# Optimization experiments

Measured on AMD Instinct MI355X. Metric: run time of the kernel, lower is better.

## Reference

```python
import jax, jax.numpy as jnp
import numpy as np

N = 170000      # nodes (ogbn-arxiv scale)
E = 2720000     # edges (avg degree 16)
IN, H, L, OUT = 128, 256, 4, 40
BN_EPS = 1e-5


def setup_inputs() -> dict:
    key = jax.random.key(0)
    ks = jax.random.split(key, 6)
    x = jax.random.normal(ks[0], (N, IN), jnp.float32)
    edge_index = jax.random.randint(ks[1], (2, E), 0, N, dtype=jnp.int64)
    W_in = jax.random.normal(ks[2], (IN, H), jnp.float32) * 0.05
    b_in = jnp.zeros((H,), jnp.float32)
    W_hid = jax.random.normal(ks[3], (L - 1, H, H), jnp.float32) * 0.05
    b_hid = jnp.zeros((L - 1, H), jnp.float32)
    gamma = jnp.ones((L, H), jnp.float32)
    beta = jnp.zeros((L, H), jnp.float32)
    W_out = jax.random.normal(ks[4], (L * H, OUT), jnp.float32) * 0.05
    b_out = jnp.zeros((OUT,), jnp.float32)
    return dict(x=x, edge_index=edge_index, W_in=W_in, b_in=b_in,
                W_hid=W_hid, b_hid=b_hid, gamma=gamma, beta=beta,
                W_out=W_out, b_out=b_out)


def _gcn_aggregate(h, src, dst, norm_e, inv_deg):
    # message passing with symmetric normalization + self-loop term
    msg = h[src] * norm_e[:, None]                      # [E, H] gather
    agg = jax.ops.segment_sum(msg, dst, num_segments=N)  # [N, H] scatter-add
    return agg + h * inv_deg[:, None]                   # self-loop: deg^-1


def reference(x, edge_index, W_in, b_in, W_hid, b_hid, gamma, beta, W_out, b_out):
    src, dst = edge_index[0], edge_index[1]
    # degree (incl. self-loop), PyG gcn_norm style
    deg = jax.ops.segment_sum(jnp.ones((E,), x.dtype), dst, num_segments=N) + 1.0
    dinv = jax.lax.rsqrt(deg)
    norm_e = dinv[src] * dinv[dst]
    inv_deg = 1.0 / deg

    outs = []
    h = x
    for i in range(L):
        W = W_in if i == 0 else W_hid[i - 1]
        b = b_in if i == 0 else b_hid[i - 1]
        h = _gcn_aggregate(h @ W, src, dst, norm_e, inv_deg) + b
        # BatchNorm1d (training-mode batch statistics, biased variance)
        mean = jnp.mean(h, axis=0)
        var = jnp.mean(jnp.square(h - mean), axis=0)
        h = (h - mean) * jax.lax.rsqrt(var + BN_EPS) * gamma[i] + beta[i]
        h = jax.nn.relu(h)  # dropout is identity in eval mode
        outs.append(h)

    z = jnp.concatenate(outs, axis=-1) @ W_out + b_out  # JK 'cat' -> [N, L*H] @ [L*H, OUT]
    return jax.nn.log_softmax(z, axis=-1)
```

## Files before the change

### kernel.cpp

```cpp
#include <hip/hip_runtime.h>
#include <math.h>

constexpr int kN = 170000;
constexpr int kE = 2720000;
constexpr int kFin = 128;
constexpr int kFh = 256;
constexpr int kL = 4;
constexpr int kFout = 40;

typedef __attribute__((ext_vector_type(8))) short bf16x8;
typedef __attribute__((ext_vector_type(4))) float f32x4;

__device__ __forceinline__ float jk_b2f(unsigned short u) {
    unsigned int x = ((unsigned int)u) << 16;
    float f;
    __builtin_memcpy(&f, &x, 4);
    return f;
}
__device__ __forceinline__ unsigned short jk_f2b(float f) {
    unsigned int x;
    __builtin_memcpy(&x, &f, 4);
    unsigned int r = (x + 0x7fffu + ((x >> 16) & 1u)) >> 16;
    return (unsigned short)r;
}

union U4 {
    uint4 v;
    unsigned short s[8];
};

__global__ void jk6_zero_i(int* p, int n) {
    int i = blockIdx.x * blockDim.x + threadIdx.x;
    if (i < n) p[i] = 0;
}
__global__ void jk6_zero_f(float* p, int n) {
    int i = blockIdx.x * blockDim.x + threadIdx.x;
    if (i < n) p[i] = 0.0f;
}

__global__ void jk6_detect(const int* eb, int* flag) {
    __shared__ int nz;
    if (threadIdx.x == 0) nz = 0;
    __syncthreads();
    int bad = 0;
    for (int j = 0; j < 4; j++) {
        int idx = threadIdx.x * 4 + j;
        if (eb[2 * idx + 1] != 0) bad = 1;
    }
    if (bad) atomicOr(&nz, 1);
    __syncthreads();
    if (threadIdx.x == 0) {
        flag[0] = nz ? 0 : 1;
        flag[1] = 0;
    }
}

__global__ void jk6_count(const int* eb, const int* flag, int* counts, int* rank) {
    int e = blockIdx.x * blockDim.x + threadIdx.x;
    if (e >= kE) return;
    int s64 = flag[0];
    int d = eb[(kE + e) << s64];
    rank[e] = atomicAdd(&counts[d], 1);
}

__global__ void jk6_nodeprep(const int* counts, float* dinv, float* invdeg, int* off,
                             int* cursor) {
    int n = blockIdx.x * blockDim.x + threadIdx.x;
    if (n < kN) {
        int c = counts[n];
        float deg = (float)c + 1.0f;
        dinv[n] = rsqrtf(deg);
        invdeg[n] = 1.0f / deg;
        off[n] = atomicAdd(cursor, c);
    }
}

__global__ void jk6_fill(const int* eb, const int* flag, const int* rank, const int* off,
                         const float* dinv, int* csr_src, float* csr_w) {
    int e = blockIdx.x * blockDim.x + threadIdx.x;
    if (e >= kE) return;
    int s64 = flag[0];
    int s = eb[e << s64];
    int d = eb[(kE + e) << s64];
    int p = off[d] + rank[e];
    csr_src[p] = s;
    csr_w[p] = dinv[s] * dinv[d];
}

__global__ void jk6_wt(const float* W, unsigned short* Wt, int K) {
    int idx = blockIdx.x * blockDim.x + threadIdx.x;
    if (idx >= K * kFh) return;
    int c = idx / K, k = idx % K;
    Wt[idx] = jk_f2b(W[(size_t)k * kFh + c]);
}

__global__ void jk6_wtout(const float* Wout, unsigned short* Wto) {
    int idx = blockIdx.x * blockDim.x + threadIdx.x;
    if (idx >= kL * 48 * 256) return;
    int l = idx / (48 * 256);
    int rem = idx % (48 * 256);
    int col = rem >> 8, k = rem & 255;
    float wv = (col < kFout) ? Wout[(size_t)(l * kFh + k) * kFout + col] : 0.f;
    unsigned short hi = jk_f2b(wv);
    float res = wv - jk_b2f(hi);
    unsigned short lo = jk_f2b(res);
    Wto[((size_t)(l * 2 + 0) * 48 + col) * 256 + k] = hi;
    Wto[((size_t)(l * 2 + 1) * 48 + col) * 256 + k] = lo;
}

template <int AF32>
__global__ __launch_bounds__(256) void jk6_gemm(const void* Aptr, const unsigned short* Wt,
                                                unsigned short* C, int K) {
    __shared__ unsigned short As[128][40];
    __shared__ unsigned short Bs[128][40];
    int tid = threadIdx.x;
    int row0 = blockIdx.x * 128;
    int n0 = blockIdx.y * 128;
    int lane = tid & 63, w = tid >> 6;
    int wm = w >> 1, wn = w & 1;
    int lr = lane & 15, lg = lane >> 4;

    f32x4 acc[4][4];
#pragma unroll
    for (int i = 0; i < 4; i++)
#pragma unroll
        for (int j = 0; j < 4; j++) acc[i][j] = (f32x4){0.f, 0.f, 0.f, 0.f};

    int sr = tid >> 1;
    int skh = (tid & 1) * 16;

    for (int k0 = 0; k0 < K; k0 += 32) {
        {
            int row = row0 + sr;
            if (AF32) {
                const float* A = (const float*)Aptr;
                unsigned short tmp[16];
                if (row < kN) {
                    const float* g = A + (size_t)row * K + k0 + skh;
#pragma unroll
                    for (int j = 0; j < 16; j++) tmp[j] = jk_f2b(g[j]);
                } else {
#pragma unroll
                    for (int j = 0; j < 16; j++) tmp[j] = 0;
                }
                *(uint4*)&As[sr][skh] = *(uint4*)&tmp[0];
                *(uint4*)&As[sr][skh + 8] = *(uint4*)&tmp[8];
            } else {
                const unsigned short* A = (const unsigned short*)Aptr;
                uint4 u0 = make_uint4(0, 0, 0, 0), u1 = make_uint4(0, 0, 0, 0);
                if (row < kN) {
                    const unsigned short* g = A + (size_t)row * K + k0 + skh;
                    u0 = *(const uint4*)g;
                    u1 = *(const uint4*)(g + 8);
                }
                *(uint4*)&As[sr][skh] = u0;
                *(uint4*)&As[sr][skh + 8] = u1;
            }
        }
        {
            const unsigned short* g = Wt + (size_t)(n0 + sr) * K + k0 + skh;
            *(uint4*)&Bs[sr][skh] = *(const uint4*)g;
            *(uint4*)&Bs[sr][skh + 8] = *(const uint4*)(g + 8);
        }
        __syncthreads();

        bf16x8 af[4], bfr[4];
#pragma unroll
        for (int mi = 0; mi < 4; mi++)
            af[mi] = *(const bf16x8*)&As[wm * 64 + mi * 16 + lr][lg * 8];
#pragma unroll
        for (int ni = 0; ni < 4; ni++)
            bfr[ni] = *(const bf16x8*)&Bs[wn * 64 + ni * 16 + lr][lg * 8];
#pragma unroll
        for (int mi = 0; mi < 4; mi++)
#pragma unroll
            for (int ni = 0; ni < 4; ni++)
                acc[mi][ni] = __builtin_amdgcn_mfma_f32_16x16x32_bf16(af[mi], bfr[ni],
                                                                      acc[mi][ni], 0, 0, 0);
        __syncthreads();
    }

#pragma unroll
    for (int mi = 0; mi < 4; mi++) {
#pragma unroll
        for (int j = 0; j < 4; j++) {
            int row = row0 + wm * 64 + mi * 16 + lg * 4 + j;
            if (row < kN) {
#pragma unroll
                for (int ni = 0; ni < 4; ni++) {
                    int col = n0 + wn * 64 + ni * 16 + lr;
                    C[(size_t)row * kFh + col] = jk_f2b(acc[mi][ni][j]);
                }
            }
        }
    }
}

__global__ __launch_bounds__(256) void jk6_agg(const unsigned short* t, const float* bias,
                                               const int* off, const int* cnt, const int* csr_src,
                                               const float* csr_w, const float* invdeg,
                                               unsigned short* h) {
    int n = blockIdx.x * 4 + (threadIdx.x >> 6);
    if (n >= kN) return;
    int l = threadIdx.x & 63;
    int half = l >> 5;
    int c0 = (l & 31) * 8;

    float acc[8];
    {
        U4 u;
        u.v = *(const uint4*)(t + (size_t)n * kFh + c0);
        float sw = half ? 0.0f : invdeg[n];
#pragma unroll
        for (int j = 0; j < 8; j++) acc[j] = sw * jk_b2f(u.s[j]);
    }

    int base = off[n], c = cnt[n];
    for (int i = 0; i < c; i += 8) {
        int e0 = i + half * 4;
        float w[4];
        U4 uu[4];
#pragma unroll
        for (int q = 0; q < 4; q++) {
            int e = e0 + q;
            bool v = e < c;
            int idx = v ? base + e : base;
            int src = csr_src[idx];
            w[q] = v ? csr_w[idx] : 0.0f;
            uu[q].v = *(const uint4*)(t + (size_t)src * kFh + c0);
        }
#pragma unroll
        for (int q = 0; q < 4; q++)
#pragma unroll
            for (int j = 0; j < 8; j++) acc[j] += w[q] * jk_b2f(uu[q].s[j]);
    }

#pragma unroll
    for (int j = 0; j < 8; j++) acc[j] += __shfl_xor(acc[j], 32, 64);

    if (half == 0) {
        U4 o;
#pragma unroll
        for (int j = 0; j < 8; j++) o.s[j] = jk_f2b(acc[j] + bias[c0 + j]);
        *(uint4*)(h + (size_t)n * kFh + c0) = o.v;
    }
}

__global__ __launch_bounds__(256) void jk6_bnstats(const unsigned short* h, float* stats) {
    __shared__ float lsum[256], lsq[256];
    int tid = threadIdx.x;
    lsum[tid] = 0.f;
    lsq[tid] = 0.f;
    __syncthreads();
    int c0 = (tid & 31) * 8;
    int grp = tid >> 5;
    float rs[8] = {}, rq[8] = {};
    for (int n = blockIdx.x * 8 + grp; n < kN; n += gridDim.x * 8) {
        U4 u;
        u.v = *(const uint4*)(h + (size_t)n * kFh + c0);
#pragma unroll
        for (int j = 0; j < 8; j++) {
            float v = jk_b2f(u.s[j]);
            rs[j] += v;
            rq[j] += v * v;
        }
    }
#pragma unroll
    for (int j = 0; j < 8; j++) {
        atomicAdd(&lsum[c0 + j], rs[j]);
        atomicAdd(&lsq[c0 + j], rq[j]);
    }
    __syncthreads();
    atomicAdd(&stats[tid], lsum[tid]);
    atomicAdd(&stats[256 + tid], lsq[tid]);
}

__global__ void jk6_bnfinal(const float* stats, const float* gamma, const float* beta, int layer,
                            float* scale, float* shift) {
    int c = threadIdx.x;
    float mean = stats[c] / (float)kN;
    float var = stats[256 + c] / (float)kN - mean * mean;
    var = var < 0.f ? 0.f : var;
    float sc = gamma[layer * kFh + c] * rsqrtf(var + 1e-5f);
    scale[c] = sc;
    shift[c] = beta[layer * kFh + c] - mean * sc;
}

template <int FIRST, int LAST>
__global__ __launch_bounds__(256) void jk6_zacc(unsigned short* h, const float* scale,
                                                const float* shift, const unsigned short* Wto,
                                                const float* bout, float* z, float* out) {
    __shared__ unsigned short Bs[2][48][264];
    __shared__ unsigned short As[128][40];
    __shared__ float ssc[256], ssh[256];
    int tid = threadIdx.x;
    for (int f = tid; f < 2 * 48 * 256; f += 256) {
        int hl = f / (48 * 256);
        int rem = f % (48 * 256);
        Bs[hl][rem >> 8][rem & 255] = Wto[f];
    }
    ssc[tid] = scale[tid];
    ssh[tid] = shift[tid];
    __syncthreads();

    int row0 = blockIdx.x * 128;
    int w = tid >> 6, lane = tid & 63;
    int lr = lane & 15, lg = lane >> 4;
    int sr = tid >> 1, skh = (tid & 1) * 16;

    f32x4 acc[2][3];
#pragma unroll
    for (int mi = 0; mi < 2; mi++)
#pragma unroll
        for (int ni = 0; ni < 3; ni++) acc[mi][ni] = (f32x4){0.f, 0.f, 0.f, 0.f};

    for (int k0 = 0; k0 < kFh; k0 += 32) {
        int row = row0 + sr;
        U4 o0, o1;
        if (row < kN) {
            U4 u0, u1;
            const unsigned short* g = h + (size_t)row * kFh + k0 + skh;
            u0.v = *(const uint4*)g;
            u1.v = *(const uint4*)(g + 8);
#pragma unroll
            for (int j = 0; j < 8; j++) {
                float v = jk_b2f(u0.s[j]) * ssc[k0 + skh + j] + ssh[k0 + skh + j];
                o0.s[j] = jk_f2b(v > 0.f ? v : 0.f);
            }
#pragma unroll
            for (int j = 0; j < 8; j++) {
                float v = jk_b2f(u1.s[j]) * ssc[k0 + skh + 8 + j] + ssh[k0 + skh + 8 + j];
                o1.s[j] = jk_f2b(v > 0.f ? v : 0.f);
            }
            if (!LAST) {
                *(uint4*)(h + (size_t)row * kFh + k0 + skh) = o0.v;
                *(uint4*)(h + (size_t)row * kFh + k0 + skh + 8) = o1.v;
            }
        } else {
#pragma unroll
            for (int j = 0; j < 8; j++) { o0.s[j] = 0; o1.s[j] = 0; }
        }
        *(uint4*)&As[sr][skh] = o0.v;
        *(uint4*)&As[sr][skh + 8] = o1.v;
        __syncthreads();

        bf16x8 af[2], bh[3], bl[3];
#pragma unroll
        for (int mi = 0; mi < 2; mi++)
            af[mi] = *(const bf16x8*)&As[w * 32 + mi * 16 + lr][lg * 8];
#pragma unroll
        for (int ni = 0; ni < 3; ni++) {
            bh[ni] = *(const bf16x8*)&Bs[0][ni * 16 + lr][k0 + lg * 8];
            bl[ni] = *(const bf16x8*)&Bs[1][ni * 16 + lr][k0 + lg * 8];
        }
#pragma unroll
        for (int mi = 0; mi < 2; mi++)
#pragma unroll
            for (int ni = 0; ni < 3; ni++) {
                acc[mi][ni] = __builtin_amdgcn_mfma_f32_16x16x32_bf16(af[mi], bh[ni],
                                                                      acc[mi][ni], 0, 0, 0);
                acc[mi][ni] = __builtin_amdgcn_mfma_f32_16x16x32_bf16(af[mi], bl[ni],
                                                                      acc[mi][ni], 0, 0, 0);
            }
        __syncthreads();
    }

#pragma unroll
    for (int mi = 0; mi < 2; mi++) {
#pragma unroll
        for (int j = 0; j < 4; j++) {
            int row = row0 + w * 32 + mi * 16 + lg * 4 + j;
            if (row >= kN) continue;
            if (!LAST) {
#pragma unroll
                for (int ni = 0; ni < 3; ni++) {
                    int col = ni * 16 + lr;
                    if (col < kFout) {
                        if (FIRST)
                            z[(size_t)row * kFout + col] = acc[mi][ni][j] + bout[col];
                        else
                            z[(size_t)row * kFout + col] += acc[mi][ni][j];
                    }
                }
            } else {
                const float* zp = z + (size_t)row * kFout;
                float v0 = zp[lr] + acc[mi][0][j];
                float v1 = zp[16 + lr] + acc[mi][1][j];
                float v2 = (lr < 8) ? (zp[32 + lr] + acc[mi][2][j]) : -1e30f;
                float m = fmaxf(fmaxf(v0, v1), v2);
                m = fmaxf(m, __shfl_xor(m, 1, 64));
                m = fmaxf(m, __shfl_xor(m, 2, 64));
                m = fmaxf(m, __shfl_xor(m, 4, 64));
                m = fmaxf(m, __shfl_xor(m, 8, 64));
                float s = expf(v0 - m) + expf(v1 - m) + ((lr < 8) ? expf(v2 - m) : 0.f);
                s += __shfl_xor(s, 1, 64);
                s += __shfl_xor(s, 2, 64);
                s += __shfl_xor(s, 4, 64);
                s += __shfl_xor(s, 8, 64);
                float ls = m + logf(s);
                float* op = out + (size_t)row * kFout;
                op[lr] = v0 - ls;
                op[16 + lr] = v1 - ls;
                if (lr < 8) op[32 + lr] = v2 - ls;
            }
        }
    }
}

extern "C" void kernel_launch(void* const* d_in, const int* in_sizes, int n_in,
                              void* d_out, int out_size, void* d_ws, size_t ws_size,
                              hipStream_t stream) {
    (void)in_sizes; (void)n_in; (void)out_size; (void)ws_size;
    const float* x = (const float*)d_in[0];
    const int* eb = (const int*)d_in[1];
    const float* W_in = (const float*)d_in[2];
    const float* b_in = (const float*)d_in[3];
    const float* W_hid = (const float*)d_in[4];
    const float* b_hid = (const float*)d_in[5];
    const float* gamma = (const float*)d_in[6];
    const float* beta = (const float*)d_in[7];
    const float* W_out = (const float*)d_in[8];
    const float* b_out = (const float*)d_in[9];
    float* out = (float*)d_out;

    char* p = (char*)d_ws;
    auto alloc = [&](size_t b) -> void* {
        void* r = (void*)p;
        p += (b + 255) & ~(size_t)255;
        return r;
    };
    int* flag = (int*)alloc(8);
    int* counts = (int*)alloc((size_t)kN * 4);
    int* off = (int*)alloc((size_t)kN * 4);
    float* dinv = (float*)alloc((size_t)kN * 4);
    float* invdeg = (float*)alloc((size_t)kN * 4);
    float* bnsums = (float*)alloc((size_t)kL * 512 * 4);
    float* bnss = (float*)alloc((size_t)kL * 512 * 4);
    int* rank = (int*)alloc((size_t)kE * 4);
    int* csr_src = (int*)alloc((size_t)kE * 4);
    float* csr_w = (float*)alloc((size_t)kE * 4);
    unsigned short* hA = (unsigned short*)alloc((size_t)kN * kFh * 2);
    unsigned short* hB = (unsigned short*)alloc((size_t)kN * kFh * 2);
    float* z = (float*)alloc((size_t)kN * kFout * 4);
    unsigned short* Wt0 = (unsigned short*)alloc((size_t)kFin * kFh * 2);
    unsigned short* Wt1 = (unsigned short*)alloc((size_t)kFh * kFh * 2);
    unsigned short* Wt2 = (unsigned short*)alloc((size_t)kFh * kFh * 2);
    unsigned short* Wt3 = (unsigned short*)alloc((size_t)kFh * kFh * 2);
    unsigned short* Wto = (unsigned short*)alloc((size_t)kL * 2 * 48 * 256 * 2);

    jk6_zero_i<<<(kN + 255) / 256, 256, 0, stream>>>(counts, kN);
    jk6_zero_f<<<(kL * 512 + 255) / 256, 256, 0, stream>>>(bnsums, kL * 512);
    jk6_detect<<<1, 256, 0, stream>>>(eb, flag);
    jk6_count<<<(kE + 255) / 256, 256, 0, stream>>>(eb, flag, counts, rank);
    jk6_nodeprep<<<(kN + 255) / 256, 256, 0, stream>>>(counts, dinv, invdeg, off, flag + 1);
    jk6_fill<<<(kE + 255) / 256, 256, 0, stream>>>(eb, flag, rank, off, dinv, csr_src, csr_w);

    jk6_wt<<<(kFin * kFh + 255) / 256, 256, 0, stream>>>(W_in, Wt0, kFin);
    jk6_wt<<<(kFh * kFh + 255) / 256, 256, 0, stream>>>(W_hid, Wt1, kFh);
    jk6_wt<<<(kFh * kFh + 255) / 256, 256, 0, stream>>>(W_hid + (size_t)kFh * kFh, Wt2, kFh);
    jk6_wt<<<(kFh * kFh + 255) / 256, 256, 0, stream>>>(W_hid + (size_t)2 * kFh * kFh, Wt3, kFh);
    jk6_wtout<<<(kL * 48 * 256 + 255) / 256, 256, 0, stream>>>(W_out, Wto);

    unsigned short* Wts[4] = {Wt0, Wt1, Wt2, Wt3};
    dim3 gg((kN + 127) / 128, 2);
    int zg = (kN + 127) / 128;
    for (int l = 0; l < kL; l++) {
        const float* b = (l == 0) ? b_in : b_hid + (size_t)(l - 1) * kFh;
        int K = (l == 0) ? kFin : kFh;
        if (l == 0)
            jk6_gemm<1><<<gg, 256, 0, stream>>>(x, Wts[l], hA, K);
        else
            jk6_gemm<0><<<gg, 256, 0, stream>>>(hB, Wts[l], hA, K);
        jk6_agg<<<(kN + 3) / 4, 256, 0, stream>>>(hA, b, off, counts, csr_src, csr_w, invdeg, hB);
        jk6_bnstats<<<1024, 256, 0, stream>>>(hB, bnsums + (size_t)l * 512);
        jk6_bnfinal<<<1, 256, 0, stream>>>(bnsums + (size_t)l * 512, gamma, beta, l,
                                           bnss + (size_t)l * 512, bnss + (size_t)l * 512 + 256);
        const unsigned short* wtl = Wto + (size_t)l * 2 * 48 * 256;
        float* sc = bnss + (size_t)l * 512;
        if (l == 0)
            jk6_zacc<1, 0><<<zg, 256, 0, stream>>>(hB, sc, sc + 256, wtl, b_out, z, out);
        else if (l < kL - 1)
            jk6_zacc<0, 0><<<zg, 256, 0, stream>>>(hB, sc, sc + 256, wtl, b_out, z, out);
        else
            jk6_zacc<0, 1><<<zg, 256, 0, stream>>>(hB, sc, sc + 256, wtl, b_out, z, out);
    }
}
```

Measured before the change: 1.802 ms.

## Fuse BN+ReLU into next GEMM load, pack CSR edges, one node per half-wave

The zacc kernel no longer writes the normalized, ReLU'd activations back to h. Instead the next layer's GEMM applies the BN scale/shift and ReLU while loading A tiles, which removes a full N×256 bf16 write per layer. Edge source index and weight are packed into one int2 array, so each edge needs a single 8-byte load. Aggregation now gives each node 32 lanes that walk all of its edges, dropping the two-half split and the cross-half shuffle reduction. This costs some extra ALU work in the GEMM prologue and gives less memory-level parallelism per node in aggregation.

```diff
diff --git a/kernel.cpp b/kernel.cpp
--- a/kernel.cpp
+++ b/kernel.cpp
@@ -29,16 +29,16 @@
     unsigned short s[8];
 };
 
-__global__ void jk6_zero_i(int* p, int n) {
+__global__ void jk7_zero_i(int* p, int n) {
     int i = blockIdx.x * blockDim.x + threadIdx.x;
     if (i < n) p[i] = 0;
 }
-__global__ void jk6_zero_f(float* p, int n) {
+__global__ void jk7_zero_f(float* p, int n) {
     int i = blockIdx.x * blockDim.x + threadIdx.x;
     if (i < n) p[i] = 0.0f;
 }
 
-__global__ void jk6_detect(const int* eb, int* flag) {
+__global__ void jk7_detect(const int* eb, int* flag) {
     __shared__ int nz;
     if (threadIdx.x == 0) nz = 0;
     __syncthreads();
@@ -55,7 +55,7 @@
     }
 }
 
-__global__ void jk6_count(const int* eb, const int* flag, int* counts, int* rank) {
+__global__ void jk7_count(const int* eb, const int* flag, int* counts, int* rank) {
     int e = blockIdx.x * blockDim.x + threadIdx.x;
     if (e >= kE) return;
     int s64 = flag[0];
@@ -63,7 +63,7 @@
     rank[e] = atomicAdd(&counts[d], 1);
 }
 
-__global__ void jk6_nodeprep(const int* counts, float* dinv, float* invdeg, int* off,
+__global__ void jk7_nodeprep(const int* counts, float* dinv, float* invdeg, int* off,
                              int* cursor) {
     int n = blockIdx.x * blockDim.x + threadIdx.x;
     if (n < kN) {
@@ -75,26 +75,26 @@
     }
 }
 
-__global__ void jk6_fill(const int* eb, const int* flag, const int* rank, const int* off,
-                         const float* dinv, int* csr_src, float* csr_w) {
+__global__ void jk7_fill(const int* eb, const int* flag, const int* rank, const int* off,
+                         const float* dinv, int2* csr) {
     int e = blockIdx.x * blockDim.x + threadIdx.x;
     if (e >= kE) return;
     int s64 = flag[0];
     int s = eb[e << s64];
     int d = eb[(kE + e) << s64];
     int p = off[d] + rank[e];
-    csr_src[p] = s;
-    csr_w[p] = dinv[s] * dinv[d];
-}
-
-__global__ void jk6_wt(const float* W, unsigned short* Wt, int K) {
+    float w = dinv[s] * dinv[d];
+    csr[p] = make_int2(s, __float_as_int(w));
+}
+
+__global__ void jk7_wt(const float* W, unsigned short* Wt, int K) {
     int idx = blockIdx.x * blockDim.x + threadIdx.x;
     if (idx >= K * kFh) return;
     int c = idx / K, k = idx % K;
     Wt[idx] = jk_f2b(W[(size_t)k * kFh + c]);
 }
 
-__global__ void jk6_wtout(const float* Wout, unsigned short* Wto) {
+__global__ void jk7_wtout(const float* Wout, unsigned short* Wto) {
     int idx = blockIdx.x * blockDim.x + threadIdx.x;
     if (idx >= kL * 48 * 256) return;
     int l = idx / (48 * 256);
@@ -108,12 +108,19 @@
     Wto[((size_t)(l * 2 + 1) * 48 + col) * 256 + k] = lo;
 }
 
-template <int AF32>
-__global__ __launch_bounds__(256) void jk6_gemm(const void* Aptr, const unsigned short* Wt,
-                                                unsigned short* C, int K) {
+template <int MODE>
+__global__ __launch_bounds__(256) void jk7_gemm(const void* Aptr, const unsigned short* Wt,
+                                                unsigned short* C, int K, const float* sc,
+                                                const float* sh) {
     __shared__ unsigned short As[128][40];
     __shared__ unsigned short Bs[128][40];
+    __shared__ float ssc[256], ssh[256];
     int tid = threadIdx.x;
+    if (MODE == 1) {
+        ssc[tid] = sc[tid];
+        ssh[tid] = sh[tid];
+    }
+    __syncthreads();
     int row0 = blockIdx.x * 128;
     int n0 = blockIdx.y * 128;
     int lane = tid & 63, w = tid >> 6;
@@ -132,7 +139,7 @@
     for (int k0 = 0; k0 < K; k0 += 32) {
         {
             int row = row0 + sr;
-            if (AF32) {
+            if (MODE == 0) {
                 const float* A = (const float*)Aptr;
                 unsigned short tmp[16];
                 if (row < kN) {
@@ -147,14 +154,28 @@
                 *(uint4*)&As[sr][skh + 8] = *(uint4*)&tmp[8];
             } else {
                 const unsigned short* A = (const unsigned short*)Aptr;
-                uint4 u0 = make_uint4(0, 0, 0, 0), u1 = make_uint4(0, 0, 0, 0);
+                U4 o0, o1;
                 if (row < kN) {
+                    U4 u0, u1;
                     const unsigned short* g = A + (size_t)row * K + k0 + skh;
-                    u0 = *(const uint4*)g;
-                    u1 = *(const uint4*)(g + 8);
+                    u0.v = *(const uint4*)g;
+                    u1.v = *(const uint4*)(g + 8);
+#pragma unroll
+                    for (int j = 0; j < 8; j++) {
+                        float v = jk_b2f(u0.s[j]) * ssc[k0 + skh + j] + ssh[k0 + skh + j];
+                        o0.s[j] = jk_f2b(v > 0.f ? v : 0.f);
+                    }
+#pragma unroll
+                    for (int j = 0; j < 8; j++) {
+                        float v = jk_b2f(u1.s[j]) * ssc[k0 + skh + 8 + j] + ssh[k0 + skh + 8 + j];
+                        o1.s[j] = jk_f2b(v > 0.f ? v : 0.f);
+                    }
+                } else {
+#pragma unroll
+                    for (int j = 0; j < 8; j++) { o0.s[j] = 0; o1.s[j] = 0; }
                 }
-                *(uint4*)&As[sr][skh] = u0;
-                *(uint4*)&As[sr][skh + 8] = u1;
+                *(uint4*)&As[sr][skh] = o0.v;
+                *(uint4*)&As[sr][skh + 8] = o1.v;
             }
         }
         {
@@ -196,38 +217,33 @@
     }
 }
 
-__global__ __launch_bounds__(256) void jk6_agg(const unsigned short* t, const float* bias,
-                                               const int* off, const int* cnt, const int* csr_src,
-                                               const float* csr_w, const float* invdeg,
-                                               unsigned short* h) {
-    int n = blockIdx.x * 4 + (threadIdx.x >> 6);
+__global__ __launch_bounds__(256) void jk7_agg(const unsigned short* t, const float* bias,
+                                               const int* off, const int* cnt, const int2* csr,
+                                               const float* invdeg, unsigned short* h) {
+    int n = blockIdx.x * 8 + (threadIdx.x >> 5);
     if (n >= kN) return;
-    int l = threadIdx.x & 63;
-    int half = l >> 5;
-    int c0 = (l & 31) * 8;
+    int c0 = (threadIdx.x & 31) * 8;
 
     float acc[8];
     {
         U4 u;
         u.v = *(const uint4*)(t + (size_t)n * kFh + c0);
-        float sw = half ? 0.0f : invdeg[n];
+        float sw = invdeg[n];
 #pragma unroll
         for (int j = 0; j < 8; j++) acc[j] = sw * jk_b2f(u.s[j]);
     }
 
     int base = off[n], c = cnt[n];
-    for (int i = 0; i < c; i += 8) {
-        int e0 = i + half * 4;
+    for (int i = 0; i < c; i += 4) {
         float w[4];
         U4 uu[4];
 #pragma unroll
         for (int q = 0; q < 4; q++) {
-            int e = e0 + q;
+            int e = i + q;
             bool v = e < c;
-            int idx = v ? base + e : base;
-            int src = csr_src[idx];
-            w[q] = v ? csr_w[idx] : 0.0f;
-            uu[q].v = *(const uint4*)(t + (size_t)src * kFh + c0);
+            int2 cw = csr[v ? base + e : base];
+            w[q] = v ? __int_as_float(cw.y) : 0.0f;
+            uu[q].v = *(const uint4*)(t + (size_t)cw.x * kFh + c0);
         }
 #pragma unroll
         for (int q = 0; q < 4; q++)
@@ -235,18 +251,13 @@
             for (int j = 0; j < 8; j++) acc[j] += w[q] * jk_b2f(uu[q].s[j]);
     }
 
-#pragma unroll
-    for (int j = 0; j < 8; j++) acc[j] += __shfl_xor(acc[j], 32, 64);
-
-    if (half == 0) {
-        U4 o;
-#pragma unroll
-        for (int j = 0; j < 8; j++) o.s[j] = jk_f2b(acc[j] + bias[c0 + j]);
-        *(uint4*)(h + (size_t)n * kFh + c0) = o.v;
-    }
-}
-
-__global__ __launch_bounds__(256) void jk6_bnstats(const unsigned short* h, float* stats) {
+    U4 o;
+#pragma unroll
+    for (int j = 0; j < 8; j++) o.s[j] = jk_f2b(acc[j] + bias[c0 + j]);
+    *(uint4*)(h + (size_t)n * kFh + c0) = o.v;
+}
+
+__global__ __launch_bounds__(256) void jk7_bnstats(const unsigned short* h, float* stats) {
     __shared__ float lsum[256], lsq[256];
     int tid = threadIdx.x;
     lsum[tid] = 0.f;
@@ -275,7 +286,7 @@
     atomicAdd(&stats[256 + tid], lsq[tid]);
 }
 
-__global__ void jk6_bnfinal(const float* stats, const float* gamma, const float* beta, int layer,
+__global__ void jk7_bnfinal(const float* stats, const float* gamma, const float* beta, int layer,
                             float* scale, float* shift) {
     int c = threadIdx.x;
     float mean = stats[c] / (float)kN;
@@ -287,7 +298,7 @@
 }
 
 template <int FIRST, int LAST>
-__global__ __launch_bounds__(256) void jk6_zacc(unsigned short* h, const float* scale,
+__global__ __launch_bounds__(256) void jk7_zacc(const unsigned short* h, const float* scale,
                                                 const float* shift, const unsigned short* Wto,
                                                 const float* bout, float* z, float* out) {
     __shared__ unsigned short Bs[2][48][264];
@@ -331,10 +342,6 @@
             for (int j = 0; j < 8; j++) {
                 float v = jk_b2f(u1.s[j]) * ssc[k0 + skh + 8 + j] + ssh[k0 + skh + 8 + j];
                 o1.s[j] = jk_f2b(v > 0.f ? v : 0.f);
-            }
-            if (!LAST) {
-                *(uint4*)(h + (size_t)row * kFh + k0 + skh) = o0.v;
-                *(uint4*)(h + (size_t)row * kFh + k0 + skh + 8) = o1.v;
             }
         } else {
 #pragma unroll
@@ -437,8 +444,7 @@
     float* bnsums = (float*)alloc((size_t)kL * 512 * 4);
     float* bnss = (float*)alloc((size_t)kL * 512 * 4);
     int* rank = (int*)alloc((size_t)kE * 4);
-    int* csr_src = (int*)alloc((size_t)kE * 4);
-    float* csr_w = (float*)alloc((size_t)kE * 4);
+    int2* csr = (int2*)alloc((size_t)kE * 8);
     unsigned short* hA = (unsigned short*)alloc((size_t)kN * kFh * 2);
     unsigned short* hB = (unsigned short*)alloc((size_t)kN * kFh * 2);
     float* z = (float*)alloc((size_t)kN * kFout * 4);
@@ -448,18 +454,18 @@
     unsigned short* Wt3 = (unsigned short*)alloc((size_t)kFh * kFh * 2);
     unsigned short* Wto = (unsigned short*)alloc((size_t)kL * 2 * 48 * 256 * 2);
 
-    jk6_zero_i<<<(kN + 255) / 256, 256, 0, stream>>>(counts, kN);
-    jk6_zero_f<<<(kL * 512 + 255) / 256, 256, 0, stream>>>(bnsums, kL * 512);
-    jk6_detect<<<1, 256, 0, stream>>>(eb, flag);
-    jk6_count<<<(kE + 255) / 256, 256, 0, stream>>>(eb, flag, counts, rank);
-    jk6_nodeprep<<<(kN + 255) / 256, 256, 0, stream>>>(counts, dinv, invdeg, off, flag + 1);
-    jk6_fill<<<(kE + 255) / 256, 256, 0, stream>>>(eb, flag, rank, off, dinv, csr_src, csr_w);
-
-    jk6_wt<<<(kFin * kFh + 255) / 256, 256, 0, stream>>>(W_in, Wt0, kFin);
-    jk6_wt<<<(kFh * kFh + 255) / 256, 256, 0, stream>>>(W_hid, Wt1, kFh);
-    jk6_wt<<<(kFh * kFh + 255) / 256, 256, 0, stream>>>(W_hid + (size_t)kFh * kFh, Wt2, kFh);
-    jk6_wt<<<(kFh * kFh + 255) / 256, 256, 0, stream>>>(W_hid + (size_t)2 * kFh * kFh, Wt3, kFh);
-    jk6_wtout<<<(kL * 48 * 256 + 255) / 256, 256, 0, stream>>>(W_out, Wto);
+    jk7_zero_i<<<(kN + 255) / 256, 256, 0, stream>>>(counts, kN);
+    jk7_zero_f<<<(kL * 512 + 255) / 256, 256, 0, stream>>>(bnsums, kL * 512);
+    jk7_detect<<<1, 256, 0, stream>>>(eb, flag);
+    jk7_count<<<(kE + 255) / 256, 256, 0, stream>>>(eb, flag, counts, rank);
+    jk7_nodeprep<<<(kN + 255) / 256, 256, 0, stream>>>(counts, dinv, invdeg, off, flag + 1);
+    jk7_fill<<<(kE + 255) / 256, 256, 0, stream>>>(eb, flag, rank, off, dinv, csr);
+
+    jk7_wt<<<(kFin * kFh + 255) / 256, 256, 0, stream>>>(W_in, Wt0, kFin);
+    jk7_wt<<<(kFh * kFh + 255) / 256, 256, 0, stream>>>(W_hid, Wt1, kFh);
+    jk7_wt<<<(kFh * kFh + 255) / 256, 256, 0, stream>>>(W_hid + (size_t)kFh * kFh, Wt2, kFh);
+    jk7_wt<<<(kFh * kFh + 255) / 256, 256, 0, stream>>>(W_hid + (size_t)2 * kFh * kFh, Wt3, kFh);
+    jk7_wtout<<<(kL * 48 * 256 + 255) / 256, 256, 0, stream>>>(W_out, Wto);
 
     unsigned short* Wts[4] = {Wt0, Wt1, Wt2, Wt3};
     dim3 gg((kN + 127) / 128, 2);
@@ -467,21 +473,23 @@
     for (int l = 0; l < kL; l++) {
         const float* b = (l == 0) ? b_in : b_hid + (size_t)(l - 1) * kFh;
         int K = (l == 0) ? kFin : kFh;
-        if (l == 0)
-            jk6_gemm<1><<<gg, 256, 0, stream>>>(x, Wts[l], hA, K);
-        else
-            jk6_gemm<0><<<gg, 256, 0, stream>>>(hB, Wts[l], hA, K);
-        jk6_agg<<<(kN + 3) / 4, 256, 0, stream>>>(hA, b, off, counts, csr_src, csr_w, invdeg, hB);
-        jk6_bnstats<<<1024, 256, 0, stream>>>(hB, bnsums + (size_t)l * 512);
-        jk6_bnfinal<<<1, 256, 0, stream>>>(bnsums + (size_t)l * 512, gamma, beta, l,
+        if (l == 0) {
+            jk7_gemm<0><<<gg, 256, 0, stream>>>(x, Wts[l], hA, K, nullptr, nullptr);
+        } else {
+            float* scp = bnss + (size_t)(l - 1) * 512;
+            jk7_gemm<1><<<gg, 256, 0, stream>>>(hB, Wts[l], hA, K, scp, scp + 256);
+        }
+        jk7_agg<<<(kN + 7) / 8, 256, 0, stream>>>(hA, b, off, counts, csr, invdeg, hB);
+        jk7_bnstats<<<1024, 256, 0, stream>>>(hB, bnsums + (size_t)l * 512);
+        jk7_bnfinal<<<1, 256, 0, stream>>>(bnsums + (size_t)l * 512, gamma, beta, l,
                                            bnss + (size_t)l * 512, bnss + (size_t)l * 512 + 256);
         const unsigned short* wtl = Wto + (size_t)l * 2 * 48 * 256;
         float* sc = bnss + (size_t)l * 512;
         if (l == 0)
-            jk6_zacc<1, 0><<<zg, 256, 0, stream>>>(hB, sc, sc + 256, wtl, b_out, z, out);
+            jk7_zacc<1, 0><<<zg, 256, 0, stream>>>(hB, sc, sc + 256, wtl, b_out, z, out);
         else if (l < kL - 1)
-            jk6_zacc<0, 0><<<zg, 256, 0, stream>>>(hB, sc, sc + 256, wtl, b_out, z, out);
+            jk7_zacc<0, 0><<<zg, 256, 0, stream>>>(hB, sc, sc + 256, wtl, b_out, z, out);
         else
-            jk6_zacc<0, 1><<<zg, 256, 0, stream>>>(hB, sc, sc + 256, wtl, b_out, z, out);
-    }
-}
+            jk7_zacc<0, 1><<<zg, 256, 0, stream>>>(hB, sc, sc + 256, wtl, b_out, z, out);
+    }
+}
```

After: 1.759 ms. 2.4% less time.
